# Kernel tuning notes

Measured on AMD Instinct MI355X. Metric: run time of the kernel, lower is better.

The kernel has to match this reference:

```python
import jax, jax.numpy as jnp
import numpy as np

EPS = 0.05
ITERS = 10


def setup_inputs() -> dict:
    key = jax.random.key(0)
    k1, k2, k3 = jax.random.split(key, 3)
    x = jax.random.normal(k1, (32, 768, 32, 32), jnp.float32)          # [B,C,H,W]
    conv_w = jax.random.normal(k2, (384, 768), jnp.float32) * 0.02     # 1x1 conv kernel [D,C]
    conv_b = jnp.zeros((384,), jnp.float32)
    v = jax.random.normal(k3, (64, 384), jnp.float32)                  # cluster codebook [K,D]
    return {"x": x, "conv_w": conv_w, "conv_b": conv_b, "v": v}


def log_sinkhorn_iterations(Z, log_mu, log_nu, iters):
    # Z: [B,M,N]; log_mu: [B,M]; log_nu: [B,N]
    u0 = jnp.zeros_like(log_mu)
    v0 = jnp.zeros_like(log_nu)

    def step(carry, _):
        u, v = carry
        u = log_mu - jax.nn.logsumexp(Z + v[:, None, :], axis=2)
        v = log_nu - jax.nn.logsumexp(Z + u[:, :, None], axis=1)
        return (u, v), None

    (u, v), _ = jax.lax.scan(step, (u0, v0), None, length=iters)
    return Z + u[:, :, None] + v[:, None, :]


def log_optimal_transport(scores, eps, iters):
    b, m, n = scores.shape
    norm = -jnp.log(jnp.asarray(float(m + n), scores.dtype))
    log_mu = jnp.full((b, m), norm, scores.dtype)
    log_nu = jnp.full((b, n), norm, scores.dtype)
    Z = log_sinkhorn_iterations(scores / eps, log_mu, log_nu, iters)
    return jnp.exp(Z - norm)


def reference(x, conv_w, conv_b, v):
    b, c, h, w = x.shape
    d = conv_w.shape[0]
    # 1x1 conv projection, then flatten spatial and move channels last: [B, HW, D]
    x_proj = jnp.einsum('bchw,dc->bhwd', x, conv_w).reshape(b, h * w, d) + conv_b
    # l2_normalize tokens
    xn = x_proj / jnp.maximum(jnp.linalg.norm(x_proj, axis=-1, keepdims=True), 1e-12)
    # normalized cluster codebook (torch does this under no_grad + in-place copy)
    clusters = v / jnp.maximum(jnp.linalg.norm(v, axis=-1, keepdims=True), 1e-12)  # [K,D]
    # cluster scores: [B, HW, K]
    scores = jnp.einsum('bnd,kd->bnk', xn, clusters)
    # OT on transposed scores [B,K,HW], transpose weights back to [B,HW,K]
    weights = jnp.transpose(
        log_optimal_transport(jnp.transpose(scores, (0, 2, 1)), EPS, ITERS), (0, 2, 1))
    # v_tilde = (x^T @ weights)^T : [B, K, D]
    v_tilde = jnp.einsum('bnd,bnk->bkd', xn, weights)
    return (v_tilde, x_proj)
```

## Files before the change

kernel.cpp:

```cpp
#include <hip/hip_runtime.h>
#include <math.h>

#define BB 32
#define CC 768
#define HWN 1024
#define DD 384
#define KK 64
#define EPSI 20.0f
#define NORMC (-6.9920964f)
#define NITERS 10

typedef __bf16 bf16;
typedef bf16 bf16x8 __attribute__((ext_vector_type(8)));
typedef bf16 bf16x4 __attribute__((ext_vector_type(4)));
typedef float f32x4 __attribute__((ext_vector_type(4)));
typedef _Float16 f16;
typedef f16 f16x2 __attribute__((ext_vector_type(2)));
typedef f16 f16x4 __attribute__((ext_vector_type(4)));

__device__ __forceinline__ float wave_sum(float v){
  #pragma unroll
  for (int off = 32; off; off >>= 1) v += __shfl_xor(v, off, 64);
  return v;
}
__device__ __forceinline__ float wave_max(float v){
  #pragma unroll
  for (int off = 32; off; off >>= 1) v = fmaxf(v, __shfl_xor(v, off, 64));
  return v;
}

__device__ __forceinline__ void async16(const bf16* g, bf16* l){
  __builtin_amdgcn_global_load_lds((const __attribute__((address_space(1))) unsigned int*)g,
                                   (__attribute__((address_space(3))) unsigned int*)l,
                                   16, 0, 0);
}

__global__ __launch_bounds__(256) void k0_clusters(const float* __restrict__ vin,
                                                   float* __restrict__ clus){
  int w = threadIdx.x >> 6, l = threadIdx.x & 63;
  int k = blockIdx.x * 4 + w;
  float s = 0.f;
  #pragma unroll
  for (int i = 0; i < 6; i++){ float x = vin[k*DD + l + 64*i]; s += x*x; }
  s = wave_sum(s);
  float scale = 1.f / fmaxf(sqrtf(s), 1e-12f);
  #pragma unroll
  for (int i = 0; i < 6; i++) clus[k*DD + l + 64*i] = vin[k*DD + l + 64*i] * scale;
}

__global__ __launch_bounds__(256) void k_wconv(const float* __restrict__ w,
                                               bf16* __restrict__ wb){
  int i = (blockIdx.x * 256 + threadIdx.x) * 4;
  float4 v = *(const float4*)&w[i];
  bf16x4 o;
  o[0] = (bf16)v.x; o[1] = (bf16)v.y; o[2] = (bf16)v.z; o[3] = (bf16)v.w;
  *(bf16x4*)&wb[i] = o;
}

__global__ __launch_bounds__(256) void k_xt(const float* __restrict__ x,
                                            bf16* __restrict__ xt){
  __shared__ float S[64][68];
  int b  = blockIdx.z;
  int k0 = blockIdx.y * 64;
  int n0 = blockIdx.x * 64;
  const float* X = x + (size_t)b * CC * HWN;
  int t = threadIdx.x;
  int rr = t >> 4, cc = (t & 15) * 4;
  #pragma unroll
  for (int it = 0; it < 4; it++){
    float4 v = *(const float4*)&X[(size_t)(k0 + rr + it*16)*HWN + n0 + cc];
    *(float4*)&S[rr + it*16][cc] = v;
  }
  __syncthreads();
  int n = t >> 2, kc = t & 3;
  bf16* orow = xt + (size_t)b * HWN * CC + (size_t)(n0 + n) * CC + k0;
  #pragma unroll
  for (int half = 0; half < 2; half++){
    int kb = half*32 + kc*8;
    bf16x8 o;
    #pragma unroll
    for (int jj = 0; jj < 8; jj++){
      int j = (jj + kc) & 7;
      o[j] = (bf16)S[kb + j][n];
    }
    *(bf16x8*)&orow[kb] = o;
  }
}

__global__ __launch_bounds__(256) void k_gemm(const bf16* __restrict__ Wb,
                                              const bf16* __restrict__ Xt,
                                              const float* __restrict__ bias,
                                              float* __restrict__ xp){
  __shared__ bf16 Wl[4][128][8];
  __shared__ bf16 Xl[4][128][8];
  int b  = blockIdx.z;
  int m0 = blockIdx.y * 128;
  int n0 = blockIdx.x * 128;
  int t = threadIdx.x, wv = t >> 6, l = t & 63;
  int l15 = l & 15, quad = l >> 4;
  int wn = wv >> 1, wm = wv & 1;
  const bf16* Xb = Xt + (size_t)b * HWN * CC;

  int kqA = wv >> 1;
  int rb  = (wv & 1) * 64;
  const bf16* gW0 = Wb + (size_t)(m0 + rb + l) * CC + kqA * 8;
  const bf16* gX0 = Xb + (size_t)(n0 + rb + l) * CC + kqA * 8;
  bf16* lW0 = &Wl[0][0][0] + wv * 512;
  bf16* lX0 = &Xl[0][0][0] + wv * 512;

  f32x4 acc[4][4];
  const f32x4 zero = {0.f, 0.f, 0.f, 0.f};
  #pragma unroll
  for (int i = 0; i < 4; i++)
    #pragma unroll
    for (int j = 0; j < 4; j++) acc[i][j] = zero;

  for (int k0 = 0; k0 < CC; k0 += 32){
    async16(gW0 + k0,      lW0);
    async16(gW0 + k0 + 16, lW0 + 2048);
    async16(gX0 + k0,      lX0);
    async16(gX0 + k0 + 16, lX0 + 2048);
    __syncthreads();
    bf16x8 xf[4], wf[4];
    #pragma unroll
    for (int i = 0; i < 4; i++)
      xf[i] = *(const bf16x8*)&Xl[quad][wn*64 + i*16 + l15][0];
    #pragma unroll
    for (int j = 0; j < 4; j++)
      wf[j] = *(const bf16x8*)&Wl[quad][wm*64 + j*16 + l15][0];
    #pragma unroll
    for (int i = 0; i < 4; i++)
      #pragma unroll
      for (int j = 0; j < 4; j++)
        acc[i][j] = __builtin_amdgcn_mfma_f32_16x16x32_bf16(xf[i], wf[j], acc[i][j], 0, 0, 0);
    __syncthreads();
  }

  float bb[4];
  #pragma unroll
  for (int j = 0; j < 4; j++) bb[j] = bias[m0 + wm*64 + j*16 + l15];
  #pragma unroll
  for (int i = 0; i < 4; i++){
    int nb = n0 + wn*64 + i*16 + quad*4;
    #pragma unroll
    for (int r = 0; r < 4; r++){
      float* orow = xp + ((size_t)b * HWN + nb + r) * DD;
      #pragma unroll
      for (int j = 0; j < 4; j++){
        int m = m0 + wm*64 + j*16 + l15;
        orow[m] = acc[i][j][r] + bb[j];
      }
    }
  }
}

__global__ __launch_bounds__(256) void k2_rnorm(const float* __restrict__ xp,
                                                float* __restrict__ rn){
  int w = threadIdx.x >> 6, l = threadIdx.x & 63;
  int t = blockIdx.x * 4 + w;
  const float* row = xp + (size_t)t * DD;
  float s = 0.f;
  #pragma unroll
  for (int i = 0; i < 6; i++){ float xv = row[l + 64*i]; s += xv*xv; }
  s = wave_sum(s);
  if (l == 0) rn[t] = 1.f / fmaxf(sqrtf(s), 1e-12f);
}

__global__ __launch_bounds__(256) void k_xpt(const float* __restrict__ xp,
                                             const float* __restrict__ rn,
                                             bf16* __restrict__ xpt){
  __shared__ float S[64][68];
  int b  = blockIdx.z;
  int d0 = blockIdx.y * 64;
  int n0 = blockIdx.x * 64;
  const float* xpb = xp + (size_t)b * HWN * DD;
  const float* rnb = rn + (size_t)b * HWN;
  int t = threadIdx.x;
  int rr = t >> 4, cc = (t & 15) * 4;
  #pragma unroll
  for (int it = 0; it < 4; it++){
    int row = rr + it*16;
    float sc = rnb[n0 + row];
    float4 v = *(const float4*)&xpb[(size_t)(n0 + row)*DD + d0 + cc];
    v.x *= sc; v.y *= sc; v.z *= sc; v.w *= sc;
    *(float4*)&S[row][cc] = v;
  }
  __syncthreads();
  int d = t >> 2, c0 = (t & 3) * 16;
  bf16* orow = xpt + (size_t)b * DD * HWN + (size_t)(d0 + d) * HWN + n0 + c0;
  bf16x8 o0, o1;
  #pragma unroll
  for (int jj = 0; jj < 8; jj++) o0[jj] = (bf16)S[c0 + jj][d];
  #pragma unroll
  for (int jj = 0; jj < 8; jj++) o1[jj] = (bf16)S[c0 + 8 + jj][d];
  *(bf16x8*)&orow[0] = o0;
  *(bf16x8*)&orow[8] = o1;
}

__global__ __launch_bounds__(256) void k3_scores(const float* __restrict__ clus,
                                                 const float* __restrict__ xp,
                                                 const float* __restrict__ rn,
                                                 float* __restrict__ Z){
  __shared__ float As[16][68];
  __shared__ float Bs[16][68];
  int b = blockIdx.y, n0 = blockIdx.x * 64;
  const float* xpb = xp + (size_t)b * HWN * DD;
  int tid = threadIdx.x, ty = tid >> 4, tx = tid & 15;
  float acc[4][4] = {};
  for (int d0 = 0; d0 < DD; d0 += 16){
    {
      int k = tid >> 2, q = tid & 3;
      const float4 a4 = *(const float4*)&clus[(size_t)k*DD + d0 + q*4];
      As[q*4+0][k] = a4.x; As[q*4+1][k] = a4.y; As[q*4+2][k] = a4.z; As[q*4+3][k] = a4.w;
    }
    {
      int nn = tid >> 2, q = tid & 3;
      const float4 x4 = *(const float4*)&xpb[(size_t)(n0+nn)*DD + d0 + q*4];
      Bs[q*4+0][nn] = x4.x; Bs[q*4+1][nn] = x4.y; Bs[q*4+2][nn] = x4.z; Bs[q*4+3][nn] = x4.w;
    }
    __syncthreads();
    #pragma unroll
    for (int kk = 0; kk < 16; kk++){
      const float4 a4 = *(const float4*)&As[kk][ty*4];
      const float4 b4 = *(const float4*)&Bs[kk][tx*4];
      const float av[4] = {a4.x, a4.y, a4.z, a4.w};
      const float bv[4] = {b4.x, b4.y, b4.z, b4.w};
      #pragma unroll
      for (int i = 0; i < 4; i++)
        #pragma unroll
        for (int j = 0; j < 4; j++)
          acc[i][j] = fmaf(av[i], bv[j], acc[i][j]);
    }
    __syncthreads();
  }
  const float* rnb = rn + (size_t)b * HWN;
  #pragma unroll
  for (int i = 0; i < 4; i++){
    int k = ty*4 + i;
    int n = n0 + tx*4;
    float4 o;
    o.x = acc[i][0] * rnb[n+0] * EPSI;
    o.y = acc[i][1] * rnb[n+1] * EPSI;
    o.z = acc[i][2] * rnb[n+2] * EPSI;
    o.w = acc[i][3] * rnb[n+3] * EPSI;
    *(float4*)&Z[((size_t)b*KK + k)*HWN + n] = o;
  }
}

__global__ __launch_bounds__(1024) void k4_sinkhorn(const float* __restrict__ Z,
                                                    float* __restrict__ U,
                                                    float* __restrict__ V){
  __shared__ f16  E[64][1024];
  __shared__ float evf[1024];
  __shared__ float eu[64];
  __shared__ float rmax[64];
  __shared__ float u_l[64];
  __shared__ float v_l[1024];
  __shared__ float sp[2][1024];
  int b = blockIdx.x;
  const float* Zb = Z + (size_t)b * KK * HWN;
  int t = threadIdx.x, w = t >> 6, l = t & 63;

  #pragma unroll
  for (int rr = 0; rr < 4; rr++){
    int r = w*4 + rr;
    float4 z[4];
    float mx = -INFINITY;
    #pragma unroll
    for (int j = 0; j < 4; j++){
      z[j] = *(const float4*)&Zb[(size_t)r*HWN + 4*l + 256*j];
      mx = fmaxf(mx, fmaxf(fmaxf(z[j].x, z[j].y), fmaxf(z[j].z, z[j].w)));
    }
    mx = wave_max(mx);
    if (l == 0) rmax[r] = mx;
    #pragma unroll
    for (int j = 0; j < 4; j++){
      f16x4 e4;
      e4[0] = (f16)__expf(z[j].x - mx); e4[1] = (f16)__expf(z[j].y - mx);
      e4[2] = (f16)__expf(z[j].z - mx); e4[3] = (f16)__expf(z[j].w - mx);
      *(f16x4*)&E[r][4*l + 256*j] = e4;
    }
  }
  evf[t] = 1.f;
  v_l[t] = 0.f;
  __syncthreads();

  for (int it = 0; it < NITERS; it++){
    float evx[16];
    #pragma unroll
    for (int j = 0; j < 8; j++){
      float2 e2 = *(const float2*)&evf[2*(l + 64*j)];
      evx[2*j] = e2.x; evx[2*j+1] = e2.y;
    }
    float us[4];
    #pragma unroll
    for (int rr = 0; rr < 4; rr++){
      int r = w*4 + rr;
      float s = 0.f;
      #pragma unroll
      for (int j = 0; j < 8; j++){
        f16x2 e2 = *(const f16x2*)&E[r][2*(l + 64*j)];
        s = fmaf((float)e2[0], evx[2*j],   s);
        s = fmaf((float)e2[1], evx[2*j+1], s);
      }
      us[rr] = wave_sum(s);
    }
    if (l == 0){
      #pragma unroll
      for (int rr = 0; rr < 4; rr++){
        int r = w*4 + rr;
        u_l[r] = NORMC - rmax[r] - __logf(us[rr]);
        eu[r]  = __expf(NORMC) / us[rr];
      }
    }
    __syncthreads();
    {
      int p = t & 511, h = t >> 9;
      float sx = 0.f, sy = 0.f;
      #pragma unroll
      for (int mq = 0; mq < 8; mq++){
        float4 eu4 = *(const float4*)&eu[h*32 + mq*4];
        const float euv[4] = {eu4.x, eu4.y, eu4.z, eu4.w};
        #pragma unroll
        for (int i = 0; i < 4; i++){
          f16x2 e2 = *(const f16x2*)&E[h*32 + mq*4 + i][2*p];
          sx = fmaf((float)e2[0], euv[i], sx);
          sy = fmaf((float)e2[1], euv[i], sy);
        }
      }
      float2 o; o.x = sx; o.y = sy;
      *(float2*)&sp[h][2*p] = o;
    }
    __syncthreads();
    if (t < 512){
      int p = t;
      float2 a = *(const float2*)&sp[0][2*p];
      float2 c = *(const float2*)&sp[1][2*p];
      float vx = NORMC - __logf(a.x + c.x);
      float vy = NORMC - __logf(a.y + c.y);
      v_l[2*p]   = vx;
      v_l[2*p+1] = vy;
      float2 ee; ee.x = __expf(vx); ee.y = __expf(vy);
      *(float2*)&evf[2*p] = ee;
    }
    __syncthreads();
  }
  V[b*HWN + t] = v_l[t];
  if (t < 64) U[b*KK + t] = u_l[t];
}

__global__ __launch_bounds__(256) void k5_mfma(const float* __restrict__ Z,
                                               const float* __restrict__ U,
                                               const float* __restrict__ V,
                                               const bf16* __restrict__ XpT,
                                               float* __restrict__ out){
  __shared__ bf16 El[64][40];
  __shared__ bf16 Xl[384][40];
  int b  = blockIdx.y;
  int nsb = blockIdx.x * 128;
  const float* Zb = Z + (size_t)b * KK * HWN;
  const bf16*  Xb = XpT + (size_t)b * DD * HWN;
  const float* Vb = V + (size_t)b * HWN;
  int t = threadIdx.x, wv = t >> 6, l = t & 63;
  int l15 = l & 15, quad = l >> 4;
  int er = t >> 2, ec0 = (t & 3) * 8;
  float ur = U[b*KK + er];

  f32x4 acc[4][6];
  const f32x4 zero = {0.f, 0.f, 0.f, 0.f};
  #pragma unroll
  for (int i = 0; i < 4; i++)
    #pragma unroll
    for (int j = 0; j < 6; j++) acc[i][j] = zero;

  for (int st = 0; st < 4; st++){
    int n0 = nsb + st*32;
    {
      float4 z0 = *(const float4*)&Zb[(size_t)er*HWN + n0 + ec0];
      float4 z1 = *(const float4*)&Zb[(size_t)er*HWN + n0 + ec0 + 4];
      float4 v0 = *(const float4*)&Vb[n0 + ec0];
      float4 v1 = *(const float4*)&Vb[n0 + ec0 + 4];
      bf16x8 e;
      e[0] = (bf16)__expf(z0.x + ur + v0.x - NORMC);
      e[1] = (bf16)__expf(z0.y + ur + v0.y - NORMC);
      e[2] = (bf16)__expf(z0.z + ur + v0.z - NORMC);
      e[3] = (bf16)__expf(z0.w + ur + v0.w - NORMC);
      e[4] = (bf16)__expf(z1.x + ur + v1.x - NORMC);
      e[5] = (bf16)__expf(z1.y + ur + v1.y - NORMC);
      e[6] = (bf16)__expf(z1.z + ur + v1.z - NORMC);
      e[7] = (bf16)__expf(z1.w + ur + v1.w - NORMC);
      *(bf16x8*)&El[er][ec0] = e;
    }
    #pragma unroll
    for (int ii = 0; ii < 6; ii++){
      int chunk = t + 256*ii;
      int d = chunk >> 2, cb = (chunk & 3) * 8;
      bf16x8 xv = *(const bf16x8*)&Xb[(size_t)d*HWN + n0 + cb];
      *(bf16x8*)&Xl[d][cb] = xv;
    }
    __syncthreads();
    bf16x8 af[4], bfr[6];
    #pragma unroll
    for (int i = 0; i < 4; i++)
      af[i] = *(const bf16x8*)&El[i*16 + l15][quad*8];
    #pragma unroll
    for (int j = 0; j < 6; j++)
      bfr[j] = *(const bf16x8*)&Xl[wv*96 + j*16 + l15][quad*8];
    #pragma unroll
    for (int i = 0; i < 4; i++)
      #pragma unroll
      for (int j = 0; j < 6; j++)
        acc[i][j] = __builtin_amdgcn_mfma_f32_16x16x32_bf16(af[i], bfr[j], acc[i][j], 0, 0, 0);
    __syncthreads();
  }

  float* ob = out + (size_t)b * KK * DD;
  #pragma unroll
  for (int i = 0; i < 4; i++){
    int kbase = i*16 + quad*4;
    #pragma unroll
    for (int j = 0; j < 6; j++){
      int d = wv*96 + j*16 + l15;
      #pragma unroll
      for (int r = 0; r < 4; r++)
        unsafeAtomicAdd(&ob[(size_t)(kbase + r)*DD + d], acc[i][j][r]);
    }
  }
}

extern "C" void kernel_launch(void* const* d_in, const int* in_sizes, int n_in,
                              void* d_out, int out_size, void* d_ws, size_t ws_size,
                              hipStream_t stream) {
  const float* x      = (const float*)d_in[0];
  const float* conv_w = (const float*)d_in[1];
  const float* conv_b = (const float*)d_in[2];
  const float* vcode  = (const float*)d_in[3];
  float* out = (float*)d_out;
  float* vt_out = out;
  float* xp_out = out + 786432;

  bf16* Xt   = (bf16*)d_ws;
  bf16* Wb   = Xt + (size_t)BB * HWN * CC;
  float* clus = (float*)(Wb + (size_t)DD * CC);
  float* Zbuf = clus + 24576;
  float* Ubuf = Zbuf + 2097152;
  float* Vbuf = Ubuf + 2048;
  float* Rn   = Vbuf + 32768;
  bf16* XpT  = Xt;

  hipMemsetAsync(vt_out, 0, (size_t)786432 * sizeof(float), stream);
  k0_clusters<<<16, 256, 0, stream>>>(vcode, clus);
  k_wconv<<<288, 256, 0, stream>>>(conv_w, Wb);
  k_xt<<<dim3(16, 12, 32), 256, 0, stream>>>(x, Xt);
  k_gemm<<<dim3(8, 3, 32), 256, 0, stream>>>(Wb, Xt, conv_b, xp_out);
  k2_rnorm<<<8192, 256, 0, stream>>>(xp_out, Rn);
  k_xpt<<<dim3(16, 6, 32), 256, 0, stream>>>(xp_out, Rn, XpT);
  k3_scores<<<dim3(16, 32), 256, 0, stream>>>(clus, xp_out, Rn, Zbuf);
  k4_sinkhorn<<<32, 1024, 0, stream>>>(Zbuf, Ubuf, Vbuf);
  k5_mfma<<<dim3(8, 32), 256, 0, stream>>>(Zbuf, Ubuf, Vbuf, XpT, vt_out);
}
```

Baseline: 335.9 us.

## Move cluster scores to bf16 MFMA and widen projection GEMM tiles

The cluster-score kernel now runs bf16 MFMA instead of fp32 FMA. It reads a bf16 normalized codebook and a bf16 normalized-token buffer, which the transpose kernel now writes as an extra output. The projection GEMM is restructured so each 512-thread block covers all 384 output channels for 128 tokens, so the X tile is loaded once per block rather than three times. This costs extra bf16 writes in k_xpt and lower precision in the scores, which are scaled by 20 before Sinkhorn.

```diff
diff --git a/kernel.cpp b/kernel.cpp
--- a/kernel.cpp
+++ b/kernel.cpp
@@ -36,7 +36,7 @@
 }
 
 __global__ __launch_bounds__(256) void k0_clusters(const float* __restrict__ vin,
-                                                   float* __restrict__ clus){
+                                                   bf16* __restrict__ clusb){
   int w = threadIdx.x >> 6, l = threadIdx.x & 63;
   int k = blockIdx.x * 4 + w;
   float s = 0.f;
@@ -45,7 +45,7 @@
   s = wave_sum(s);
   float scale = 1.f / fmaxf(sqrtf(s), 1e-12f);
   #pragma unroll
-  for (int i = 0; i < 6; i++) clus[k*DD + l + 64*i] = vin[k*DD + l + 64*i] * scale;
+  for (int i = 0; i < 6; i++) clusb[k*DD + l + 64*i] = (bf16)(vin[k*DD + l + 64*i] * scale);
 }
 
 __global__ __launch_bounds__(256) void k_wconv(const float* __restrict__ w,
@@ -87,58 +87,57 @@
   }
 }
 
-__global__ __launch_bounds__(256) void k_gemm(const bf16* __restrict__ Wb,
+__global__ __launch_bounds__(512) void k_gemm(const bf16* __restrict__ Wb,
                                               const bf16* __restrict__ Xt,
                                               const float* __restrict__ bias,
                                               float* __restrict__ xp){
-  __shared__ bf16 Wl[4][128][8];
-  __shared__ bf16 Xl[4][128][8];
-  int b  = blockIdx.z;
-  int m0 = blockIdx.y * 128;
+  __shared__ bf16 Wl[384][4][8];
+  __shared__ bf16 Xl[128][4][8];
+  int b  = blockIdx.y;
   int n0 = blockIdx.x * 128;
   int t = threadIdx.x, wv = t >> 6, l = t & 63;
   int l15 = l & 15, quad = l >> 4;
-  int wn = wv >> 1, wm = wv & 1;
+  int wn = wv >> 2, wm = wv & 3;
   const bf16* Xb = Xt + (size_t)b * HWN * CC;
 
-  int kqA = wv >> 1;
-  int rb  = (wv & 1) * 64;
-  const bf16* gW0 = Wb + (size_t)(m0 + rb + l) * CC + kqA * 8;
-  const bf16* gX0 = Xb + (size_t)(n0 + rb + l) * CC + kqA * 8;
-  bf16* lW0 = &Wl[0][0][0] + wv * 512;
-  bf16* lX0 = &Xl[0][0][0] + wv * 512;
-
-  f32x4 acc[4][4];
+  int rbase = wv*16 + (l >> 2);
+  int kq8   = (l & 3) * 8;
+  const bf16* gX = Xb + (size_t)(n0 + rbase) * CC + kq8;
+  const bf16* gW = Wb + (size_t)rbase * CC + kq8;
+  bf16* lX = &Xl[0][0][0] + wv * 512;
+  bf16* lW = &Wl[0][0][0] + wv * 512;
+
+  f32x4 acc[4][6];
   const f32x4 zero = {0.f, 0.f, 0.f, 0.f};
   #pragma unroll
   for (int i = 0; i < 4; i++)
     #pragma unroll
-    for (int j = 0; j < 4; j++) acc[i][j] = zero;
+    for (int j = 0; j < 6; j++) acc[i][j] = zero;
 
   for (int k0 = 0; k0 < CC; k0 += 32){
-    async16(gW0 + k0,      lW0);
-    async16(gW0 + k0 + 16, lW0 + 2048);
-    async16(gX0 + k0,      lX0);
-    async16(gX0 + k0 + 16, lX0 + 2048);
-    __syncthreads();
-    bf16x8 xf[4], wf[4];
-    #pragma unroll
-    for (int i = 0; i < 4; i++)
-      xf[i] = *(const bf16x8*)&Xl[quad][wn*64 + i*16 + l15][0];
-    #pragma unroll
-    for (int j = 0; j < 4; j++)
-      wf[j] = *(const bf16x8*)&Wl[quad][wm*64 + j*16 + l15][0];
-    #pragma unroll
-    for (int i = 0; i < 4; i++)
-      #pragma unroll
-      for (int j = 0; j < 4; j++)
+    async16(gX + k0, lX);
+    async16(gW + k0,                  lW);
+    async16(gW + k0 + (size_t)128*CC, lW + 4096);
+    async16(gW + k0 + (size_t)256*CC, lW + 8192);
+    __syncthreads();
+    bf16x8 xf[4], wf[6];
+    #pragma unroll
+    for (int i = 0; i < 4; i++)
+      xf[i] = *(const bf16x8*)&Xl[wn*64 + i*16 + l15][quad][0];
+    #pragma unroll
+    for (int j = 0; j < 6; j++)
+      wf[j] = *(const bf16x8*)&Wl[wm*96 + j*16 + l15][quad][0];
+    #pragma unroll
+    for (int i = 0; i < 4; i++)
+      #pragma unroll
+      for (int j = 0; j < 6; j++)
         acc[i][j] = __builtin_amdgcn_mfma_f32_16x16x32_bf16(xf[i], wf[j], acc[i][j], 0, 0, 0);
     __syncthreads();
   }
 
-  float bb[4];
-  #pragma unroll
-  for (int j = 0; j < 4; j++) bb[j] = bias[m0 + wm*64 + j*16 + l15];
+  float bb[6];
+  #pragma unroll
+  for (int j = 0; j < 6; j++) bb[j] = bias[wm*96 + j*16 + l15];
   #pragma unroll
   for (int i = 0; i < 4; i++){
     int nb = n0 + wn*64 + i*16 + quad*4;
@@ -146,10 +145,8 @@
     for (int r = 0; r < 4; r++){
       float* orow = xp + ((size_t)b * HWN + nb + r) * DD;
       #pragma unroll
-      for (int j = 0; j < 4; j++){
-        int m = m0 + wm*64 + j*16 + l15;
-        orow[m] = acc[i][j][r] + bb[j];
-      }
+      for (int j = 0; j < 6; j++)
+        orow[wm*96 + j*16 + l15] = acc[i][j][r] + bb[j];
     }
   }
 }
@@ -168,7 +165,8 @@
 
 __global__ __launch_bounds__(256) void k_xpt(const float* __restrict__ xp,
                                              const float* __restrict__ rn,
-                                             bf16* __restrict__ xpt){
+                                             bf16* __restrict__ xpt,
+                                             bf16* __restrict__ xnb){
   __shared__ float S[64][68];
   int b  = blockIdx.z;
   int d0 = blockIdx.y * 64;
@@ -184,6 +182,9 @@
     float4 v = *(const float4*)&xpb[(size_t)(n0 + row)*DD + d0 + cc];
     v.x *= sc; v.y *= sc; v.z *= sc; v.w *= sc;
     *(float4*)&S[row][cc] = v;
+    bf16x4 o4;
+    o4[0] = (bf16)v.x; o4[1] = (bf16)v.y; o4[2] = (bf16)v.z; o4[3] = (bf16)v.w;
+    *(bf16x4*)&xnb[((size_t)b * HWN + n0 + row)*DD + d0 + cc] = o4;
   }
   __syncthreads();
   int d = t >> 2, c0 = (t & 3) * 16;
@@ -197,53 +198,58 @@
   *(bf16x8*)&orow[8] = o1;
 }
 
-__global__ __launch_bounds__(256) void k3_scores(const float* __restrict__ clus,
-                                                 const float* __restrict__ xp,
-                                                 const float* __restrict__ rn,
+__global__ __launch_bounds__(256) void k3_scores(const bf16* __restrict__ clusb,
+                                                 const bf16* __restrict__ xnb,
                                                  float* __restrict__ Z){
-  __shared__ float As[16][68];
-  __shared__ float Bs[16][68];
-  int b = blockIdx.y, n0 = blockIdx.x * 64;
-  const float* xpb = xp + (size_t)b * HWN * DD;
-  int tid = threadIdx.x, ty = tid >> 4, tx = tid & 15;
-  float acc[4][4] = {};
-  for (int d0 = 0; d0 < DD; d0 += 16){
-    {
-      int k = tid >> 2, q = tid & 3;
-      const float4 a4 = *(const float4*)&clus[(size_t)k*DD + d0 + q*4];
-      As[q*4+0][k] = a4.x; As[q*4+1][k] = a4.y; As[q*4+2][k] = a4.z; As[q*4+3][k] = a4.w;
-    }
-    {
-      int nn = tid >> 2, q = tid & 3;
-      const float4 x4 = *(const float4*)&xpb[(size_t)(n0+nn)*DD + d0 + q*4];
-      Bs[q*4+0][nn] = x4.x; Bs[q*4+1][nn] = x4.y; Bs[q*4+2][nn] = x4.z; Bs[q*4+3][nn] = x4.w;
-    }
-    __syncthreads();
-    #pragma unroll
-    for (int kk = 0; kk < 16; kk++){
-      const float4 a4 = *(const float4*)&As[kk][ty*4];
-      const float4 b4 = *(const float4*)&Bs[kk][tx*4];
-      const float av[4] = {a4.x, a4.y, a4.z, a4.w};
-      const float bv[4] = {b4.x, b4.y, b4.z, b4.w};
-      #pragma unroll
-      for (int i = 0; i < 4; i++)
-        #pragma unroll
-        for (int j = 0; j < 4; j++)
-          acc[i][j] = fmaf(av[i], bv[j], acc[i][j]);
-    }
-    __syncthreads();
-  }
-  const float* rnb = rn + (size_t)b * HWN;
+  __shared__ bf16 Al[64][4][8];
+  __shared__ bf16 Bl[128][4][8];
+  int b = blockIdx.y, n0 = blockIdx.x * 128;
+  const bf16* Xb = xnb + (size_t)b * HWN * DD;
+  int t = threadIdx.x, wv = t >> 6, l = t & 63;
+  int l15 = l & 15, quad = l >> 4;
+
+  int rbase = wv*16 + (l >> 2);
+  int kq8   = (l & 3) * 8;
+  const bf16* gA = clusb + (size_t)rbase * DD + kq8;
+  const bf16* gB = Xb + (size_t)(n0 + rbase) * DD + kq8;
+  bf16* lA = &Al[0][0][0] + wv * 512;
+  bf16* lB = &Bl[0][0][0] + wv * 512;
+
+  f32x4 acc[4][2];
+  const f32x4 zero = {0.f, 0.f, 0.f, 0.f};
+  #pragma unroll
+  for (int i = 0; i < 4; i++){ acc[i][0] = zero; acc[i][1] = zero; }
+
+  for (int d0 = 0; d0 < DD; d0 += 32){
+    async16(gA + d0, lA);
+    async16(gB + d0,                 lB);
+    async16(gB + d0 + (size_t)64*DD, lB + 2048);
+    __syncthreads();
+    bf16x8 af[4], bf[2];
+    #pragma unroll
+    for (int i = 0; i < 4; i++)
+      af[i] = *(const bf16x8*)&Al[i*16 + l15][quad][0];
+    #pragma unroll
+    for (int j = 0; j < 2; j++)
+      bf[j] = *(const bf16x8*)&Bl[wv*32 + j*16 + l15][quad][0];
+    #pragma unroll
+    for (int i = 0; i < 4; i++)
+      #pragma unroll
+      for (int j = 0; j < 2; j++)
+        acc[i][j] = __builtin_amdgcn_mfma_f32_16x16x32_bf16(af[i], bf[j], acc[i][j], 0, 0, 0);
+    __syncthreads();
+  }
   #pragma unroll
   for (int i = 0; i < 4; i++){
-    int k = ty*4 + i;
-    int n = n0 + tx*4;
-    float4 o;
-    o.x = acc[i][0] * rnb[n+0] * EPSI;
-    o.y = acc[i][1] * rnb[n+1] * EPSI;
-    o.z = acc[i][2] * rnb[n+2] * EPSI;
-    o.w = acc[i][3] * rnb[n+3] * EPSI;
-    *(float4*)&Z[((size_t)b*KK + k)*HWN + n] = o;
+    #pragma unroll
+    for (int j = 0; j < 2; j++){
+      int n = n0 + wv*32 + j*16 + l15;
+      #pragma unroll
+      for (int r = 0; r < 4; r++){
+        int k = i*16 + quad*4 + r;
+        Z[((size_t)b*KK + k)*HWN + n] = acc[i][j][r] * EPSI;
+      }
+    }
   }
 }
 
@@ -439,23 +445,24 @@
   float* vt_out = out;
   float* xp_out = out + 786432;
 
-  bf16* Xt   = (bf16*)d_ws;
-  bf16* Wb   = Xt + (size_t)BB * HWN * CC;
-  float* clus = (float*)(Wb + (size_t)DD * CC);
-  float* Zbuf = clus + 24576;
+  bf16* Xt    = (bf16*)d_ws;
+  bf16* Wb    = Xt + (size_t)BB * HWN * CC;
+  bf16* clusb = Wb + (size_t)DD * CC;
+  float* Zbuf = (float*)(clusb + 24576);
   float* Ubuf = Zbuf + 2097152;
   float* Vbuf = Ubuf + 2048;
   float* Rn   = Vbuf + 32768;
-  bf16* XpT  = Xt;
+  bf16* xnb   = (bf16*)(Rn + 32768);
+  bf16* XpT   = Xt;
 
   hipMemsetAsync(vt_out, 0, (size_t)786432 * sizeof(float), stream);
-  k0_clusters<<<16, 256, 0, stream>>>(vcode, clus);
+  k0_clusters<<<16, 256, 0, stream>>>(vcode, clusb);
   k_wconv<<<288, 256, 0, stream>>>(conv_w, Wb);
   k_xt<<<dim3(16, 12, 32), 256, 0, stream>>>(x, Xt);
-  k_gemm<<<dim3(8, 3, 32), 256, 0, stream>>>(Wb, Xt, conv_b, xp_out);
+  k_gemm<<<dim3(8, 32), 512, 0, stream>>>(Wb, Xt, conv_b, xp_out);
   k2_rnorm<<<8192, 256, 0, stream>>>(xp_out, Rn);
-  k_xpt<<<dim3(16, 6, 32), 256, 0, stream>>>(xp_out, Rn, XpT);
-  k3_scores<<<dim3(16, 32), 256, 0, stream>>>(clus, xp_out, Rn, Zbuf);
+  k_xpt<<<dim3(16, 6, 32), 256, 0, stream>>>(xp_out, Rn, XpT, xnb);
+  k3_scores<<<dim3(8, 32), 256, 0, stream>>>(clusb, xnb, Zbuf);
   k4_sinkhorn<<<32, 1024, 0, stream>>>(Zbuf, Ubuf, Vbuf);
   k5_mfma<<<dim3(8, 32), 256, 0, stream>>>(Zbuf, Ubuf, Vbuf, XpT, vt_out);
 }
```

Result: faster. 310.1 us (-7.7%).
